# Kernel optimization log

Measured on AMD Instinct MI355X. Metric: run time of the kernel, lower is better.

Reference implementation:

```python
import jax, jax.numpy as jnp
import numpy as np

N_NODES = 50000
N_EDGES = 800000
D_IN = 128
D_HID = 128
D_OUT = 128
N_LAYERS = 2
NEG_SLOPE = 0.2


def leaky(x):
    return jnp.where(x >= 0, x, NEG_SLOPE * x)


def setup_inputs() -> dict:
    key = jax.random.key(0)
    ks = jax.random.split(key, 12)
    s = 1.0 / np.sqrt(D_HID)
    feats = jax.random.normal(ks[0], (N_NODES, D_IN), dtype=jnp.float32)
    src = jax.random.randint(ks[1], (N_EDGES,), 0, N_NODES)
    dst = jax.random.randint(ks[2], (N_EDGES,), 0, N_NODES)
    # SIRConv params per layer: W_Q (dst), W_K (src), W_R (output proj)
    Wq = jax.random.normal(ks[3], (N_LAYERS, D_IN, D_HID), dtype=jnp.float32) * s
    bq = jnp.zeros((N_LAYERS, D_HID), dtype=jnp.float32)
    Wk = jax.random.normal(ks[4], (N_LAYERS, D_IN, D_HID), dtype=jnp.float32) * s
    bk = jnp.zeros((N_LAYERS, D_HID), dtype=jnp.float32)
    Wr = jax.random.normal(ks[5], (N_LAYERS, D_HID, D_HID), dtype=jnp.float32) * s
    br = jnp.zeros((N_LAYERS, D_HID), dtype=jnp.float32)
    # Jumping-knowledge readouts: one per entry of feats_list (input + each layer);
    # input_dim == hidden_dim so weights stack along the leading axis.
    Wro = jax.random.normal(ks[6], (N_LAYERS + 1, D_HID, D_OUT), dtype=jnp.float32) * s
    bro = jnp.zeros((N_LAYERS + 1, D_OUT), dtype=jnp.float32)
    return {"feats": feats, "Wq": Wq, "bq": bq, "Wk": Wk, "bk": bk,
            "Wr": Wr, "br": br, "Wro": Wro, "bro": bro,
            "src": src, "dst": dst}


def reference(feats, Wq, bq, Wk, bk, Wr, br, Wro, bro, src, dst):
    # mean-aggregation denominator: in-degree, clamped to 1
    deg = jax.ops.segment_sum(jnp.ones((N_EDGES,), jnp.float32), dst,
                              num_segments=N_NODES)
    denom = jnp.maximum(deg, 1.0)[:, None]  # [N, 1]

    feats_list = [feats]
    h = feats
    for i in range(N_LAYERS):
        hq = h @ Wq[i] + bq[i]          # [N, H] (dst transform)
        hk = h @ Wk[i] + bk[i]          # [N, H] (src transform)
        m = leaky(hq[dst] + hk[src])    # [E, H] contextualized messages
        agg = jax.ops.segment_sum(m, dst, num_segments=N_NODES) / denom
        h = agg @ Wr[i] + br[i]         # conv output (+ residual = 0)
        h = leaky(h)                    # norm='none', dropout=0
        feats_list.append(h)

    # jumping-knowledge readout: sum of per-stage linear readouts
    score = feats_list[0] @ Wro[0] + bro[0]
    for i in range(1, N_LAYERS + 1):
        score = score + feats_list[i] @ Wro[i] + bro[i]
    return score
```

## Files before the change

### kernel.cpp

```cpp
#include <hip/hip_runtime.h>

#define NN 50000
#define NE 800000
#define D 128
#define NEG 0.2f

#define NBLK1 256
#define TILE1 3125
#define NB2 196
#define CAP2 8192
#define NT64 782

#define SB_PREP 576
#define SB_CONV 6250
#define SB_HIST NBLK1
#define SB_TOTAL (SB_PREP + SB_CONV + SB_HIST)

typedef short bf8_t __attribute__((ext_vector_type(8)));
typedef float f4_t __attribute__((ext_vector_type(4)));

__device__ __forceinline__ unsigned short f2bf(float f) {
  unsigned int u = __float_as_uint(f);
  return (unsigned short)((u + 0x7FFF + ((u >> 16) & 1)) >> 16);
}
__device__ __forceinline__ float bf2f(unsigned int b) { return __uint_as_float(b << 16); }

__device__ __forceinline__ f4_t MF(bf8_t a, bf8_t b, f4_t c) {
  return __builtin_amdgcn_mfma_f32_16x16x32_bf16(a, b, c, 0, 0, 0);
}


__device__ __forceinline__ void stage_w(unsigned short* wbuf,
                                        const unsigned short* __restrict__ WT, int t) {
#pragma unroll
  for (int i = 0; i < 8; ++i) {
    int idx8 = t + i * 256;
    *(uint4*)(wbuf + idx8 * 8) = *(const uint4*)(WT + idx8 * 8);
  }
}

__device__ __forceinline__ void load_a16(const unsigned short* __restrict__ A,
                                         int base, int l15, int quad, bf8_t (&afr)[4]) {
  int r = base + l15;
  if (r >= NN) r = NN - 1;
  const unsigned short* p = A + (size_t)r * D + quad * 8;
#pragma unroll
  for (int kc = 0; kc < 4; ++kc) afr[kc] = *(const bf8_t*)(p + kc * 32);
}

__device__ __forceinline__ void tile16(const unsigned short* wbuf, const bf8_t (&afr)[4],
                                       int l15, int quad, f4_t (&acc)[8]) {
#pragma unroll
  for (int kc = 0; kc < 4; ++kc)
#pragma unroll
    for (int nt = 0; nt < 8; ++nt) {
      bf8_t b = *(const bf8_t*)(wbuf + (nt * 16 + l15) * D + kc * 32 + quad * 8);
      acc[nt] = MF(afr[kc], b, acc[nt]);
    }
}

__global__ __launch_bounds__(256) void setup(
    const float* __restrict__ Wq, const float* __restrict__ Wk,
    const float* __restrict__ Wr, const float* __restrict__ Wro,
    const float* __restrict__ feats, const int* __restrict__ dst,
    unsigned short* __restrict__ WT, unsigned short* __restrict__ x0,
    int* __restrict__ H) {
  __shared__ int cnt[NB2];
  const int b = blockIdx.x;
  const int t = threadIdx.x;
  if (b < SB_PREP) {
    const int m = b >> 6, xb = b & 63;
    const float* src;
    if (m < 2) src = Wq + m * D * D;
    else if (m < 4) src = Wk + (m - 2) * D * D;
    else if (m < 6) src = Wr + (m - 4) * D * D;
    else src = Wro + (m - 6) * D * D;
    const int n = xb * 2 + (t >> 7);
    const int k = t & 127;
    WT[(size_t)m * D * D + n * D + k] = f2bf(src[k * D + n]);
  } else if (b < SB_PREP + SB_CONV) {
    int i = ((b - SB_PREP) * 256 + t) * 4;
    float4 v = *(const float4*)(feats + i);
    ushort4 o = {f2bf(v.x), f2bf(v.y), f2bf(v.z), f2bf(v.w)};
    *(ushort4*)(x0 + i) = o;
  } else {
    const int blk = b - SB_PREP - SB_CONV;
    if (t < NB2) cnt[t] = 0;
    __syncthreads();
    const int beg = blk * TILE1, end = beg + TILE1;
    for (int i = beg + t; i < end; i += 256) atomicAdd(&cnt[dst[i] >> 8], 1);
    __syncthreads();
    if (t < NB2) H[t * NBLK1 + blk] = cnt[t];
  }
}

__global__ __launch_bounds__(256) void p1_scan(const int* __restrict__ H,
                                               int* __restrict__ gofs) {
  __shared__ int sd[256];
  __shared__ int wsum[4];
  const int bin = blockIdx.x;
  const int t = threadIdx.x;
  const int wave = t >> 6, lane = t & 63;
  int part = 0;
  for (int b2 = 0; b2 < bin; ++b2) part += H[b2 * NBLK1 + t];
  for (int off = 32; off; off >>= 1) part += __shfl_down(part, off, 64);
  if (lane == 0) wsum[wave] = part;
  __syncthreads();
  const int base = wsum[0] + wsum[1] + wsum[2] + wsum[3];
  int x = H[bin * NBLK1 + t];
  sd[t] = x;
  __syncthreads();
  int acc = x;
  for (int off = 1; off < 256; off <<= 1) {
    int y = (t >= off) ? sd[t - off] : 0;
    __syncthreads();
    acc += y;
    sd[t] = acc;
    __syncthreads();
  }
  gofs[bin * NBLK1 + t] = base + (acc - x);
}

__global__ __launch_bounds__(256) void p1_scatter(const int* __restrict__ src,
                                                  const int* __restrict__ dst,
                                                  const int* __restrict__ gofs,
                                                  unsigned int* __restrict__ ebuf) {
  __shared__ int lofs[NB2];
  const int t = threadIdx.x;
  const int blk = blockIdx.x;
  if (t < NB2) lofs[t] = gofs[t * NBLK1 + blk];
  __syncthreads();
  const int beg = blk * TILE1, end = beg + TILE1;
  for (int i = beg + t; i < end; i += 256) {
    unsigned int d = (unsigned int)dst[i];
    int pos = atomicAdd(&lofs[d >> 8], 1);
    ebuf[pos] = (unsigned int)src[i] | (d << 16);
  }
}

__global__ __launch_bounds__(256) void sort_qk0(
    const int* __restrict__ gofs, const unsigned int* __restrict__ ebuf,
    int* __restrict__ ssrc, int* __restrict__ rowptr, int* __restrict__ deg,
    const unsigned short* __restrict__ x0,
    const unsigned short* __restrict__ WTq, const float* __restrict__ bq_,
    const unsigned short* __restrict__ WTk, const float* __restrict__ bk_,
    unsigned short* __restrict__ hq, unsigned short* __restrict__ hk) {
  __shared__ __align__(16) unsigned char smraw[35840];
  const int t = threadIdx.x;
  const int gx = blockIdx.x;
  if (gx < NB2) {
    int* cnt = (int*)smraw;
    int* fill = cnt + 256;
    int* sd = fill + 256;
    unsigned int* sorted = (unsigned int*)(sd + 256);
    const int b = gx;
    const int beg = gofs[b * NBLK1];
    const int end = (b + 1 < NB2) ? gofs[(b + 1) * NBLK1] : NE;
    const int n = end - beg;
    cnt[t] = 0;
    __syncthreads();
    for (int i = beg + t; i < end; i += 256)
      atomicAdd(&cnt[(ebuf[i] >> 16) & 255], 1);
    __syncthreads();
    int x = cnt[t];
    sd[t] = x;
    __syncthreads();
    int acc = x;
    for (int off = 1; off < 256; off <<= 1) {
      int y = (t >= off) ? sd[t - off] : 0;
      __syncthreads();
      acc += y;
      sd[t] = acc;
      __syncthreads();
    }
    const int excl = acc - x;
    fill[t] = excl;
    __syncthreads();
    for (int i = beg + t; i < end; i += 256) {
      unsigned int p = ebuf[i];
      int pos = atomicAdd(&fill[(p >> 16) & 255], 1);
      if (pos < CAP2) sorted[pos] = p;
    }
    __syncthreads();
    for (int i = t; i < n; i += 256) ssrc[beg + i] = (int)(sorted[i] & 0xFFFFu);
    const int node = (b << 8) + t;
    if (node < NN) {
      rowptr[node] = beg + excl;
      deg[node] = x;
    }
    if (b == 0 && t == 0) rowptr[NN] = NE;
  } else {
    unsigned short* wbuf = (unsigned short*)smraw;
    const int g = gx - NB2;
    const int sel = g & 1, tile = g >> 1;
    const int wave = t >> 6, lane = t & 63;
    const int l15 = lane & 15, quad = lane >> 4;
    const int base = tile * 64 + wave * 16;
    stage_w(wbuf, sel ? WTk : WTq, t);
    bf8_t afr[4];
    load_a16(x0, base, l15, quad, afr);
    __syncthreads();
    f4_t acc[8] = {};
    tile16(wbuf, afr, l15, quad, acc);
    const float* bias = sel ? bk_ : bq_;
    unsigned short* C = sel ? hk : hq;
#pragma unroll
    for (int nt = 0; nt < 8; ++nt) {
      int col = nt * 16 + l15;
      float bb = bias[col];
#pragma unroll
      for (int reg = 0; reg < 4; ++reg) {
        int row = base + quad * 4 + reg;
        if (row < NN) C[(size_t)row * D + col] = f2bf(acc[nt][reg] + bb);
      }
    }
  }
}

#define PROC(kb)                                                     \
  {                                                                  \
    float m;                                                         \
    m = q[0] + bf2f(kb.x & 0xFFFFu); a[0] += m >= 0.f ? m : NEG * m; \
    m = q[1] + bf2f(kb.x >> 16);     a[1] += m >= 0.f ? m : NEG * m; \
    m = q[2] + bf2f(kb.y & 0xFFFFu); a[2] += m >= 0.f ? m : NEG * m; \
    m = q[3] + bf2f(kb.y >> 16);     a[3] += m >= 0.f ? m : NEG * m; \
    m = q[4] + bf2f(kb.z & 0xFFFFu); a[4] += m >= 0.f ? m : NEG * m; \
    m = q[5] + bf2f(kb.z >> 16);     a[5] += m >= 0.f ? m : NEG * m; \
    m = q[6] + bf2f(kb.w & 0xFFFFu); a[6] += m >= 0.f ? m : NEG * m; \
    m = q[7] + bf2f(kb.w >> 16);     a[7] += m >= 0.f ? m : NEG * m; \
  }

__global__ __launch_bounds__(256) void aggregate(
    const int* __restrict__ rowptr, const int* __restrict__ ssrc,
    const int* __restrict__ deg,
    const unsigned short* __restrict__ hq, const unsigned short* __restrict__ hk,
    unsigned short* __restrict__ ag) {
  const int wave = threadIdx.x >> 6, lane = threadIdx.x & 63;
  const int v = blockIdx.x * 4 + wave;
  if (v >= NN) return;
  const int sub = lane & 15, grp = lane >> 4;
  const int beg = rowptr[v], end = rowptr[v + 1];

  uint4 qb = *(const uint4*)(hq + (size_t)v * D + sub * 8);
  float q[8];
  q[0] = bf2f(qb.x & 0xFFFFu); q[1] = bf2f(qb.x >> 16);
  q[2] = bf2f(qb.y & 0xFFFFu); q[3] = bf2f(qb.y >> 16);
  q[4] = bf2f(qb.z & 0xFFFFu); q[5] = bf2f(qb.z >> 16);
  q[6] = bf2f(qb.w & 0xFFFFu); q[7] = bf2f(qb.w >> 16);

  float a[8] = {0.f, 0.f, 0.f, 0.f, 0.f, 0.f, 0.f, 0.f};
  int e = beg + grp;
  for (; e + 4 < end; e += 8) {
    int s0 = ssrc[e];
    int s1 = ssrc[e + 4];
    uint4 k0 = *(const uint4*)(hk + (size_t)s0 * D + sub * 8);
    uint4 k1 = *(const uint4*)(hk + (size_t)s1 * D + sub * 8);
    PROC(k0);
    PROC(k1);
  }
  if (e < end) {
    int s0 = ssrc[e];
    uint4 k0 = *(const uint4*)(hk + (size_t)s0 * D + sub * 8);
    PROC(k0);
  }
#pragma unroll
  for (int j = 0; j < 8; ++j) {
    a[j] += __shfl_xor(a[j], 16, 64);
    a[j] += __shfl_xor(a[j], 32, 64);
  }
  if (grp == 0) {
    float inv = 1.f / fmaxf((float)deg[v], 1.f);
    uint4 o;
    o.x = (unsigned int)f2bf(a[0] * inv) | ((unsigned int)f2bf(a[1] * inv) << 16);
    o.y = (unsigned int)f2bf(a[2] * inv) | ((unsigned int)f2bf(a[3] * inv) << 16);
    o.z = (unsigned int)f2bf(a[4] * inv) | ((unsigned int)f2bf(a[5] * inv) << 16);
    o.w = (unsigned int)f2bf(a[6] * inv) | ((unsigned int)f2bf(a[7] * inv) << 16);
    *(uint4*)(ag + (size_t)v * D + sub * 8) = o;
  }
}

template <bool LEAKY>
__global__ __launch_bounds__(256) void gemm64(const unsigned short* __restrict__ A,
                                              const unsigned short* __restrict__ WT0,
                                              const float* __restrict__ b0,
                                              unsigned short* __restrict__ C0,
                                              const unsigned short* __restrict__ WT1,
                                              const float* __restrict__ b1,
                                              unsigned short* __restrict__ C1) {
  __shared__ unsigned short wbuf[D * D];
  const int t = threadIdx.x, wave = t >> 6, lane = t & 63;
  const int l15 = lane & 15, quad = lane >> 4;
  const int sel = blockIdx.x;
  const unsigned short* WT = sel ? WT1 : WT0;
  const float* bias = sel ? b1 : b0;
  unsigned short* C = sel ? C1 : C0;
  const int base = blockIdx.y * 64 + wave * 16;

  stage_w(wbuf, WT, t);
  bf8_t afr[4];
  load_a16(A, base, l15, quad, afr);
  __syncthreads();

  f4_t acc[8] = {};
  tile16(wbuf, afr, l15, quad, acc);

#pragma unroll
  for (int nt = 0; nt < 8; ++nt) {
    int col = nt * 16 + l15;
    float b = bias[col];
#pragma unroll
    for (int reg = 0; reg < 4; ++reg) {
      int row = base + quad * 4 + reg;
      if (row < NN) {
        float v = acc[nt][reg] + b;
        if (LEAKY) v = v >= 0.f ? v : NEG * v;
        C[(size_t)row * D + col] = f2bf(v);
      }
    }
  }
}

__global__ __launch_bounds__(256) void readout(const unsigned short* __restrict__ x0,
                                               const unsigned short* __restrict__ h1,
                                               const unsigned short* __restrict__ h2,
                                               const unsigned short* __restrict__ WTro,
                                               const float* __restrict__ bro_,
                                               float* __restrict__ out) {
  __shared__ unsigned short wbuf[D * D];
  const int t = threadIdx.x, wave = t >> 6, lane = t & 63;
  const int l15 = lane & 15, quad = lane >> 4;
  const int base = blockIdx.x * 64 + wave * 16;
  const unsigned short* As[3] = {x0, h1, h2};

  f4_t acc[8] = {};
#pragma unroll
  for (int ph = 0; ph < 3; ++ph) {
    stage_w(wbuf, WTro + (size_t)ph * D * D, t);
    bf8_t afr[4];
    load_a16(As[ph], base, l15, quad, afr);
    __syncthreads();
    tile16(wbuf, afr, l15, quad, acc);
    if (ph < 2) __syncthreads();
  }

#pragma unroll
  for (int nt = 0; nt < 8; ++nt) {
    int col = nt * 16 + l15;
    float b = bro_[col] + bro_[D + col] + bro_[2 * D + col];
#pragma unroll
    for (int reg = 0; reg < 4; ++reg) {
      int row = base + quad * 4 + reg;
      if (row < NN) out[(size_t)row * D + col] = acc[nt][reg] + b;
    }
  }
}

extern "C" void kernel_launch(void* const* d_in, const int* in_sizes, int n_in,
                              void* d_out, int out_size, void* d_ws, size_t ws_size,
                              hipStream_t stream) {
  const float* feats = (const float*)d_in[0];
  const float* Wq = (const float*)d_in[1];
  const float* bq = (const float*)d_in[2];
  const float* Wk = (const float*)d_in[3];
  const float* bk = (const float*)d_in[4];
  const float* Wr = (const float*)d_in[5];
  const float* br = (const float*)d_in[6];
  const float* Wro = (const float*)d_in[7];
  const float* bro = (const float*)d_in[8];
  const int* src = (const int*)d_in[9];
  const int* dst = (const int*)d_in[10];
  float* out = (float*)d_out;

  size_t off = 0;
  char* base = (char*)d_ws;
  auto alloc = [&](size_t bytes) -> void* {
    void* p = base + off;
    off += (bytes + 255) & ~(size_t)255;
    return p;
  };
  int* H = (int*)alloc((size_t)NB2 * NBLK1 * 4);
  int* gofs = (int*)alloc((size_t)NB2 * NBLK1 * 4);
  unsigned int* ebuf = (unsigned int*)alloc((size_t)NE * 4);
  int* ssrc = (int*)alloc((size_t)NE * 4);
  int* rowptr = (int*)alloc((size_t)(NN + 1) * 4);
  int* deg = (int*)alloc((size_t)NN * 4);
  unsigned short* WT = (unsigned short*)alloc((size_t)9 * D * D * 2);
  unsigned short* x0 = (unsigned short*)alloc((size_t)NN * D * 2);
  unsigned short* hq = (unsigned short*)alloc((size_t)NN * D * 2);
  unsigned short* hk = (unsigned short*)alloc((size_t)NN * D * 2);
  unsigned short* ag = (unsigned short*)alloc((size_t)NN * D * 2);
  unsigned short* h1 = (unsigned short*)alloc((size_t)NN * D * 2);
  unsigned short* h2 = (unsigned short*)alloc((size_t)NN * D * 2);

  const size_t WM = (size_t)D * D;
  const int ab = (NN + 3) / 4;

  setup<<<SB_TOTAL, 256, 0, stream>>>(Wq, Wk, Wr, Wro, feats, dst, WT, x0, H);
  p1_scan<<<NB2, 256, 0, stream>>>(H, gofs);
  p1_scatter<<<NBLK1, 256, 0, stream>>>(src, dst, gofs, ebuf);
  sort_qk0<<<NB2 + 2 * NT64, 256, 0, stream>>>(gofs, ebuf, ssrc, rowptr, deg,
                                               x0, WT + 0 * WM, bq, WT + 2 * WM, bk,
                                               hq, hk);
  aggregate<<<ab, 256, 0, stream>>>(rowptr, ssrc, deg, hq, hk, ag);
  gemm64<true><<<dim3(1, NT64), 256, 0, stream>>>(ag, WT + 4 * WM, br, h1,
                                                  WT + 4 * WM, br, h1);
  gemm64<false><<<dim3(2, NT64), 256, 0, stream>>>(h1, WT + 1 * WM, bq + D, hq,
                                                   WT + 3 * WM, bk + D, hk);
  aggregate<<<ab, 256, 0, stream>>>(rowptr, ssrc, deg, hq, hk, ag);
  gemm64<true><<<dim3(1, NT64), 256, 0, stream>>>(ag, WT + 5 * WM, br + D, h2,
                                                  WT + 5 * WM, br + D, h2);
  readout<<<NT64, 256, 0, stream>>>(x0, h1, h2, WT + 6 * WM, bro, out);
}
```

Before: 312.3 us.

## Fuse Wr projection with next-layer Q/K and readout GEMMs, swizzle LDS, unroll gather

Merges the layer-1 output projection with the layer-2 Q/K projections into one kernel, and the layer-2 projection with the jumping-knowledge readout, keeping the intermediate activation tile in shared memory. This removes two launches plus the global write and re-read of h1 (for Q/K) and h2. LDS weight and activation layouts get an XOR swizzle to cut bank conflicts, and the aggregate gather loop is unrolled to four outstanding loads. The cost is doubled shared memory per block (lower occupancy) and more serialized weight staging inside each block.

```diff
diff --git a/kernel.cpp b/kernel.cpp
--- a/kernel.cpp
+++ b/kernel.cpp
@@ -29,13 +29,15 @@
   return __builtin_amdgcn_mfma_f32_16x16x32_bf16(a, b, c, 0, 0, 0);
 }
 
+__device__ __forceinline__ int swz_u(int u) { return u ^ ((u >> 4) & 7); }
+
 
 __device__ __forceinline__ void stage_w(unsigned short* wbuf,
                                         const unsigned short* __restrict__ WT, int t) {
 #pragma unroll
   for (int i = 0; i < 8; ++i) {
-    int idx8 = t + i * 256;
-    *(uint4*)(wbuf + idx8 * 8) = *(const uint4*)(WT + idx8 * 8);
+    int u = t + i * 256;
+    *(uint4*)(wbuf + swz_u(u) * 8) = *(const uint4*)(WT + u * 8);
   }
 }
 
@@ -48,15 +50,43 @@
   for (int kc = 0; kc < 4; ++kc) afr[kc] = *(const bf8_t*)(p + kc * 32);
 }
 
+__device__ __forceinline__ void load_a16_lds(const unsigned short* buf, int wave,
+                                             int l15, int quad, bf8_t (&afr)[4]) {
+  const int r = wave * 16 + l15;
+#pragma unroll
+  for (int kc = 0; kc < 4; ++kc)
+    afr[kc] = *(const bf8_t*)(buf + swz_u(r * 16 + kc * 4 + quad) * 8);
+}
+
 __device__ __forceinline__ void tile16(const unsigned short* wbuf, const bf8_t (&afr)[4],
                                        int l15, int quad, f4_t (&acc)[8]) {
 #pragma unroll
   for (int kc = 0; kc < 4; ++kc)
 #pragma unroll
     for (int nt = 0; nt < 8; ++nt) {
-      bf8_t b = *(const bf8_t*)(wbuf + (nt * 16 + l15) * D + kc * 32 + quad * 8);
+      bf8_t b = *(const bf8_t*)(wbuf + swz_u((nt * 16 + l15) * 16 + kc * 4 + quad) * 8);
       acc[nt] = MF(afr[kc], b, acc[nt]);
     }
+}
+
+__device__ __forceinline__ void store_c(unsigned short* __restrict__ C,
+                                        const float* __restrict__ bias,
+                                        const f4_t (&acc)[8], int base, int l15, int quad,
+                                        bool lk) {
+#pragma unroll
+  for (int nt = 0; nt < 8; ++nt) {
+    int col = nt * 16 + l15;
+    float bb = bias[col];
+#pragma unroll
+    for (int reg = 0; reg < 4; ++reg) {
+      int row = base + quad * 4 + reg;
+      if (row < NN) {
+        float v = acc[nt][reg] + bb;
+        if (lk) v = v >= 0.f ? v : NEG * v;
+        C[(size_t)row * D + col] = f2bf(v);
+      }
+    }
+  }
 }
 
 __global__ __launch_bounds__(256) void setup(
@@ -202,18 +232,7 @@
     __syncthreads();
     f4_t acc[8] = {};
     tile16(wbuf, afr, l15, quad, acc);
-    const float* bias = sel ? bk_ : bq_;
-    unsigned short* C = sel ? hk : hq;
-#pragma unroll
-    for (int nt = 0; nt < 8; ++nt) {
-      int col = nt * 16 + l15;
-      float bb = bias[col];
-#pragma unroll
-      for (int reg = 0; reg < 4; ++reg) {
-        int row = base + quad * 4 + reg;
-        if (row < NN) C[(size_t)row * D + col] = f2bf(acc[nt][reg] + bb);
-      }
-    }
+    store_c(sel ? hk : hq, sel ? bk_ : bq_, acc, base, l15, quad, false);
   }
 }
 
@@ -250,6 +269,20 @@
 
   float a[8] = {0.f, 0.f, 0.f, 0.f, 0.f, 0.f, 0.f, 0.f};
   int e = beg + grp;
+  for (; e + 12 < end; e += 16) {
+    int s0 = ssrc[e];
+    int s1 = ssrc[e + 4];
+    int s2 = ssrc[e + 8];
+    int s3 = ssrc[e + 12];
+    uint4 k0 = *(const uint4*)(hk + (size_t)s0 * D + sub * 8);
+    uint4 k1 = *(const uint4*)(hk + (size_t)s1 * D + sub * 8);
+    uint4 k2 = *(const uint4*)(hk + (size_t)s2 * D + sub * 8);
+    uint4 k3 = *(const uint4*)(hk + (size_t)s3 * D + sub * 8);
+    PROC(k0);
+    PROC(k1);
+    PROC(k2);
+    PROC(k3);
+  }
   for (; e + 4 < end; e += 8) {
     int s0 = ssrc[e];
     int s1 = ssrc[e + 4];
@@ -279,78 +312,129 @@
   }
 }
 
-template <bool LEAKY>
-__global__ __launch_bounds__(256) void gemm64(const unsigned short* __restrict__ A,
-                                              const unsigned short* __restrict__ WT0,
-                                              const float* __restrict__ b0,
-                                              unsigned short* __restrict__ C0,
-                                              const unsigned short* __restrict__ WT1,
-                                              const float* __restrict__ b1,
-                                              unsigned short* __restrict__ C1) {
+__global__ __launch_bounds__(256) void wr_qk1(
+    const unsigned short* __restrict__ ag,
+    const unsigned short* __restrict__ WTr, const float* __restrict__ brr,
+    unsigned short* __restrict__ h1,
+    const unsigned short* __restrict__ WTq, const float* __restrict__ bq1,
+    unsigned short* __restrict__ hq,
+    const unsigned short* __restrict__ WTk, const float* __restrict__ bk1,
+    unsigned short* __restrict__ hk) {
   __shared__ unsigned short wbuf[D * D];
+  __shared__ unsigned short abuf[64 * D];
   const int t = threadIdx.x, wave = t >> 6, lane = t & 63;
   const int l15 = lane & 15, quad = lane >> 4;
-  const int sel = blockIdx.x;
-  const unsigned short* WT = sel ? WT1 : WT0;
-  const float* bias = sel ? b1 : b0;
-  unsigned short* C = sel ? C1 : C0;
-  const int base = blockIdx.y * 64 + wave * 16;
-
-  stage_w(wbuf, WT, t);
+  const int tb = blockIdx.x * 64;
+  const int base = tb + wave * 16;
+
+  stage_w(wbuf, WTr, t);
   bf8_t afr[4];
-  load_a16(A, base, l15, quad, afr);
-  __syncthreads();
-
+  load_a16(ag, base, l15, quad, afr);
+  __syncthreads();
   f4_t acc[8] = {};
   tile16(wbuf, afr, l15, quad, acc);
-
 #pragma unroll
   for (int nt = 0; nt < 8; ++nt) {
     int col = nt * 16 + l15;
-    float b = bias[col];
+    float bb = brr[col];
+#pragma unroll
+    for (int reg = 0; reg < 4; ++reg) {
+      int rl = wave * 16 + quad * 4 + reg;
+      float v = acc[nt][reg] + bb;
+      v = v >= 0.f ? v : NEG * v;
+      int s = rl * D + col;
+      abuf[s ^ ((rl & 7) << 3)] = f2bf(v);
+    }
+  }
+  __syncthreads();
+
+#pragma unroll
+  for (int i = 0; i < 4; ++i) {
+    int u = t + i * 256;
+    int row = tb + (u >> 4);
+    if (row < NN)
+      *(uint4*)(h1 + (size_t)tb * D + u * 8) = *(const uint4*)(abuf + swz_u(u) * 8);
+  }
+  bf8_t hfr[4];
+  load_a16_lds(abuf, wave, l15, quad, hfr);
+
+  stage_w(wbuf, WTq, t);
+  __syncthreads();
+  f4_t accq[8] = {};
+  tile16(wbuf, hfr, l15, quad, accq);
+  store_c(hq, bq1, accq, base, l15, quad, false);
+  __syncthreads();
+
+  stage_w(wbuf, WTk, t);
+  __syncthreads();
+  f4_t acck[8] = {};
+  tile16(wbuf, hfr, l15, quad, acck);
+  store_c(hk, bk1, acck, base, l15, quad, false);
+}
+
+__global__ __launch_bounds__(256) void wr_ro(
+    const unsigned short* __restrict__ ag,
+    const unsigned short* __restrict__ WTr, const float* __restrict__ brr,
+    const unsigned short* __restrict__ x0,
+    const unsigned short* __restrict__ h1,
+    const unsigned short* __restrict__ WTro, const float* __restrict__ bro_,
+    float* __restrict__ out) {
+  __shared__ unsigned short wbuf[D * D];
+  __shared__ unsigned short abuf[64 * D];
+  const int t = threadIdx.x, wave = t >> 6, lane = t & 63;
+  const int l15 = lane & 15, quad = lane >> 4;
+  const int tb = blockIdx.x * 64;
+  const int base = tb + wave * 16;
+
+  stage_w(wbuf, WTr, t);
+  bf8_t afr[4];
+  load_a16(ag, base, l15, quad, afr);
+  __syncthreads();
+  f4_t acch[8] = {};
+  tile16(wbuf, afr, l15, quad, acch);
+#pragma unroll
+  for (int nt = 0; nt < 8; ++nt) {
+    int col = nt * 16 + l15;
+    float bb = brr[col];
+#pragma unroll
+    for (int reg = 0; reg < 4; ++reg) {
+      int rl = wave * 16 + quad * 4 + reg;
+      float v = acch[nt][reg] + bb;
+      v = v >= 0.f ? v : NEG * v;
+      int s = rl * D + col;
+      abuf[s ^ ((rl & 7) << 3)] = f2bf(v);
+    }
+  }
+  __syncthreads();
+
+  bf8_t hfr[4];
+  load_a16_lds(abuf, wave, l15, quad, hfr);
+  f4_t acc[8] = {};
+
+  stage_w(wbuf, WTro + 2 * (size_t)D * D, t);
+  __syncthreads();
+  tile16(wbuf, hfr, l15, quad, acc);
+  __syncthreads();
+
+  stage_w(wbuf, WTro, t);
+  load_a16(x0, base, l15, quad, afr);
+  __syncthreads();
+  tile16(wbuf, afr, l15, quad, acc);
+  __syncthreads();
+
+  stage_w(wbuf, WTro + (size_t)D * D, t);
+  load_a16(h1, base, l15, quad, afr);
+  __syncthreads();
+  tile16(wbuf, afr, l15, quad, acc);
+
+#pragma unroll
+  for (int nt = 0; nt < 8; ++nt) {
+    int col = nt * 16 + l15;
+    float bsum = bro_[col] + bro_[D + col] + bro_[2 * D + col];
 #pragma unroll
     for (int reg = 0; reg < 4; ++reg) {
       int row = base + quad * 4 + reg;
-      if (row < NN) {
-        float v = acc[nt][reg] + b;
-        if (LEAKY) v = v >= 0.f ? v : NEG * v;
-        C[(size_t)row * D + col] = f2bf(v);
-      }
-    }
-  }
-}
-
-__global__ __launch_bounds__(256) void readout(const unsigned short* __restrict__ x0,
-                                               const unsigned short* __restrict__ h1,
-                                               const unsigned short* __restrict__ h2,
-                                               const unsigned short* __restrict__ WTro,
-                                               const float* __restrict__ bro_,
-                                               float* __restrict__ out) {
-  __shared__ unsigned short wbuf[D * D];
-  const int t = threadIdx.x, wave = t >> 6, lane = t & 63;
-  const int l15 = lane & 15, quad = lane >> 4;
-  const int base = blockIdx.x * 64 + wave * 16;
-  const unsigned short* As[3] = {x0, h1, h2};
-
-  f4_t acc[8] = {};
-#pragma unroll
-  for (int ph = 0; ph < 3; ++ph) {
-    stage_w(wbuf, WTro + (size_t)ph * D * D, t);
-    bf8_t afr[4];
-    load_a16(As[ph], base, l15, quad, afr);
-    __syncthreads();
-    tile16(wbuf, afr, l15, quad, acc);
-    if (ph < 2) __syncthreads();
-  }
-
-#pragma unroll
-  for (int nt = 0; nt < 8; ++nt) {
-    int col = nt * 16 + l15;
-    float b = bro_[col] + bro_[D + col] + bro_[2 * D + col];
-#pragma unroll
-    for (int reg = 0; reg < 4; ++reg) {
-      int row = base + quad * 4 + reg;
-      if (row < NN) out[(size_t)row * D + col] = acc[nt][reg] + b;
+      if (row < NN) out[(size_t)row * D + col] = acc[nt][reg] + bsum;
     }
   }
 }
@@ -390,7 +474,6 @@
   unsigned short* hk = (unsigned short*)alloc((size_t)NN * D * 2);
   unsigned short* ag = (unsigned short*)alloc((size_t)NN * D * 2);
   unsigned short* h1 = (unsigned short*)alloc((size_t)NN * D * 2);
-  unsigned short* h2 = (unsigned short*)alloc((size_t)NN * D * 2);
 
   const size_t WM = (size_t)D * D;
   const int ab = (NN + 3) / 4;
@@ -402,12 +485,10 @@
                                                x0, WT + 0 * WM, bq, WT + 2 * WM, bk,
                                                hq, hk);
   aggregate<<<ab, 256, 0, stream>>>(rowptr, ssrc, deg, hq, hk, ag);
-  gemm64<true><<<dim3(1, NT64), 256, 0, stream>>>(ag, WT + 4 * WM, br, h1,
-                                                  WT + 4 * WM, br, h1);
-  gemm64<false><<<dim3(2, NT64), 256, 0, stream>>>(h1, WT + 1 * WM, bq + D, hq,
-                                                   WT + 3 * WM, bk + D, hk);
+  wr_qk1<<<NT64, 256, 0, stream>>>(ag, WT + 4 * WM, br, h1,
+                                   WT + 1 * WM, bq + D, hq,
+                                   WT + 3 * WM, bk + D, hk);
   aggregate<<<ab, 256, 0, stream>>>(rowptr, ssrc, deg, hq, hk, ag);
-  gemm64<true><<<dim3(1, NT64), 256, 0, stream>>>(ag, WT + 5 * WM, br + D, h2,
-                                                  WT + 5 * WM, br + D, h2);
-  readout<<<NT64, 256, 0, stream>>>(x0, h1, h2, WT + 6 * WM, bro, out);
-}
+  wr_ro<<<NT64, 256, 0, stream>>>(ag, WT + 5 * WM, br + D, x0, h1,
+                                  WT + 6 * WM, bro, out);
+}
```

Measured after the change: 284.6 us. -8.9%, faster.
